# Optimization experiments

Measured on AMD Instinct MI355X. Metric: run time of the kernel, lower is better.

The kernel has to match this reference:

```python
import jax, jax.numpy as jnp
import numpy as np

N, D, H, O, E = 8192, 512, 2048, 512, 8

def setup_inputs() -> dict:
    key = jax.random.key(0)
    ks = jax.random.split(key, 7)
    s = lambda *sh: 1.0 / np.sqrt(sh[-2] if len(sh) > 1 else 1.0)
    x  = jax.random.normal(ks[0], (N, D), dtype=jnp.float32)
    Wr = jax.random.normal(ks[1], (D, E), dtype=jnp.float32) * (1.0 / np.sqrt(D))
    br = jnp.zeros((E,), dtype=jnp.float32)
    W1 = jax.random.normal(ks[2], (E, D, H), dtype=jnp.float32) * (1.0 / np.sqrt(D))
    b1 = jnp.zeros((E, H), dtype=jnp.float32)
    W2 = jax.random.normal(ks[3], (E, H, O), dtype=jnp.float32) * (1.0 / np.sqrt(H))
    b2 = jnp.zeros((E, O), dtype=jnp.float32)
    return {"x": x, "Wr": Wr, "br": br, "W1": W1, "b1": b1, "W2": W2, "b2": b2}


def reference(x, Wr, br, W1, b1, W2, b2):
    # --- supervised router step: Linear -> softmax -> max ---
    router_logits = x @ Wr + br                      # [N, E]
    router_probs = jax.nn.softmax(router_logits, axis=-1)
    p_max = jnp.max(router_probs, axis=-1)           # [N]
    routes = jnp.argmax(router_probs, axis=-1)       # [N] int
    onehot = jax.nn.one_hot(routes, W1.shape[0], dtype=x.dtype)  # [N, E] dispatch mask

    # --- per-expert MLP (dense reference for the gather/compute/scatter pattern) ---
    h = jax.nn.relu(jnp.einsum('nd,edh->enh', x, W1) + b1[:, None, :])  # [E, N, H]
    all_out = jnp.einsum('enh,eho->eno', h, W2) + b2[:, None, :]        # [E, N, O]

    # --- combine: each token takes its routed expert's output ---
    out = jnp.einsum('ne,eno->no', onehot, all_out)  # [N, O]

    # straight-through scaling: value 1 in fwd, routes gradient into router probs
    scale = p_max / jax.lax.stop_gradient(p_max)
    logits = out * scale[:, None]

    counts = jnp.sum(onehot, axis=0)                 # tokens per expert
    return logits, router_probs, counts
```

## Files before the change

### kernel.cpp

```cpp
#include <hip/hip_runtime.h>
#include <hip/hip_bf16.h>
#include <stdint.h>

#define N_TOK 8192
#define DIM   512
#define HID   2048
#define OUTD  512
#define NEXP  8

typedef short  bf16x8 __attribute__((ext_vector_type(8)));
typedef float  f32x4  __attribute__((ext_vector_type(4)));
typedef unsigned short u16x8 __attribute__((ext_vector_type(8)));

#define WS_CNT    0
#define WS_LIST   4096
#define WS_XBF    266240
#define WS_W1T    8654848
#define WS_W2T    25432064
#define WS_H      42209280

__device__ __forceinline__ unsigned short f2bf(float f) {
    uint32_t u = __builtin_bit_cast(uint32_t, f);
    u = (u + 0x7fffu + ((u >> 16) & 1u)) >> 16;
    return (unsigned short)u;
}

__device__ __forceinline__ void gload16(const void* g, void* l) {
    __builtin_amdgcn_global_load_lds(
        (const __attribute__((address_space(1))) unsigned int*)g,
        (__attribute__((address_space(3))) unsigned int*)l, 16, 0, 0);
}

#define MFMA_BF16 __builtin_amdgcn_mfma_f32_16x16x32_bf16

__global__ __launch_bounds__(256) void k1_kernel(
    const float* __restrict__ x, const float* __restrict__ wr, const float* __restrict__ br,
    const float* __restrict__ w1,
    float* __restrict__ probs, int* __restrict__ cnt, int* __restrict__ list,
    unsigned short* __restrict__ xbf, unsigned short* __restrict__ w1t)
{
    const int bid = blockIdx.x, tid = threadIdx.x;
    if (bid < 256) {
        __shared__ int lcnt[NEXP], lbase[NEXP];
        __shared__ int am_l[32], slot_l[32];
        const int w = tid >> 6, lane = tid & 63;
        if (tid < NEXP) lcnt[tid] = 0;
        __syncthreads();
        for (int i = 0; i < 8; i++) {
            const int n = bid * 32 + w * 8 + i;
            float acc[NEXP] = {};
            #pragma unroll
            for (int db = 0; db < 8; db++) {
                const int d = db * 64 + lane;
                const float xv = x[(size_t)n * DIM + d];
                const f32x4 wv0 = *(const f32x4*)&wr[d * 8];
                const f32x4 wv1 = *(const f32x4*)&wr[d * 8 + 4];
                #pragma unroll
                for (int e = 0; e < 4; e++) { acc[e] += xv * wv0[e]; acc[4 + e] += xv * wv1[e]; }
            }
            #pragma unroll
            for (int m = 1; m < 64; m <<= 1)
                #pragma unroll
                for (int e = 0; e < NEXP; e++) acc[e] += __shfl_xor(acc[e], m, 64);
            #pragma unroll
            for (int e = 0; e < NEXP; e++) acc[e] += br[e];
            float mx = acc[0]; int am = 0;
            #pragma unroll
            for (int e = 1; e < NEXP; e++) if (acc[e] > mx) { mx = acc[e]; am = e; }
            float p[NEXP]; float s = 0.f;
            #pragma unroll
            for (int e = 0; e < NEXP; e++) { p[e] = expf(acc[e] - mx); s += p[e]; }
            const float inv = 1.f / s;
            if (lane == 0) {
                f32x4 p0, p1;
                #pragma unroll
                for (int e = 0; e < 4; e++) { p0[e] = p[e] * inv; p1[e] = p[e + 4] * inv; }
                *(f32x4*)&probs[(size_t)n * NEXP]     = p0;
                *(f32x4*)&probs[(size_t)n * NEXP + 4] = p1;
                const int slot = atomicAdd(&lcnt[am], 1);
                am_l[w * 8 + i] = am; slot_l[w * 8 + i] = slot;
            }
        }
        __syncthreads();
        if (tid < NEXP) lbase[tid] = atomicAdd(&cnt[tid], lcnt[tid]);
        __syncthreads();
        if (tid < 32) {
            const int a = am_l[tid];
            list[a * N_TOK + lbase[a] + slot_l[tid]] = bid * 32 + tid;
        }
        const int row = bid * 32 + (tid >> 3), seg = tid & 7;
        const float* src = x + (size_t)row * DIM + seg * 64;
        unsigned short* dst = xbf + (size_t)row * DIM + seg * 64;
        #pragma unroll
        for (int j = 0; j < 8; j++) {
            f32x4 a = *(const f32x4*)&src[j * 8];
            f32x4 b = *(const f32x4*)&src[j * 8 + 4];
            u16x8 o;
            #pragma unroll
            for (int q2 = 0; q2 < 4; q2++) { o[q2] = f2bf(a[q2]); o[4 + q2] = f2bf(b[q2]); }
            *(u16x8*)&dst[j * 8] = o;
        }
    } else {
        __shared__ float t[64][65];
        const int loc = bid - 256, e = loc >> 8, l2 = loc & 255;
        const float* pin = w1 + (size_t)e * DIM * HID;
        unsigned short* pout = w1t + (size_t)e * DIM * HID;
        const int r0 = (l2 >> 5) * 64, c0 = (l2 & 31) * 64;
        const int r = tid >> 2, q = tid & 3;
        #pragma unroll
        for (int j = 0; j < 4; j++) {
            f32x4 v = *(const f32x4*)&pin[(size_t)(r0 + r) * HID + c0 + q * 16 + j * 4];
            #pragma unroll
            for (int i = 0; i < 4; i++) t[r][q * 16 + j * 4 + i] = v[i];
        }
        __syncthreads();
        unsigned short o[16];
        #pragma unroll
        for (int i = 0; i < 16; i++) o[i] = f2bf(t[q * 16 + i][r]);
        unsigned short* dst = &pout[(size_t)(c0 + r) * DIM + r0 + q * 16];
        *(u16x8*)dst       = *(const u16x8*)&o[0];
        *(u16x8*)(dst + 8) = *(const u16x8*)&o[8];
    }
}

__device__ __forceinline__ int xcd_swizzle(int bid, int nwg, bool& valid) {
    const int xcd = bid & 7, cidx = bid >> 3;
    const int q = nwg >> 3, r = nwg & 7;
    const int csz = q + (xcd < r ? 1 : 0);
    valid = (cidx < csz);
    return (xcd < r ? xcd * (q + 1) : r * (q + 1) + (xcd - r) * q) + cidx;
}

__device__ __forceinline__ void tile_map128(const int* __restrict__ cnt, int tile,
                                            int& e, int& row0, int& bs, int& m_e, int& ntiles) {
    int c[NEXP]; ntiles = 0;
    #pragma unroll
    for (int i = 0; i < NEXP; i++) { c[i] = cnt[i]; ntiles += (c[i] + 127) >> 7; }
    int t = tile, b = 0, ei = 0;
    #pragma unroll
    for (int i = 0; i < NEXP; i++) {
        const int nt = (c[i] + 127) >> 7;
        if (t >= 0 && t < nt) { ei = i; row0 = t << 7; bs = b; m_e = c[i]; }
        t -= nt; b += c[i];
    }
    e = ei;
}

#define G1_TILES 2272

__global__ __launch_bounds__(256) void gemmB_kernel(
    const unsigned short* __restrict__ xbf, const unsigned short* __restrict__ w1t,
    const float* __restrict__ b1, const int* __restrict__ list,
    const int* __restrict__ cnt, unsigned short* __restrict__ h,
    const float* __restrict__ w2, unsigned short* __restrict__ w2t)
{
    __shared__ char smem[25088] __attribute__((aligned(16)));
    const int bid = blockIdx.x, tid = threadIdx.x;
    int role, idx;
    if (bid < 4096) { role = (bid >> 3) & 1; idx = ((bid >> 4) << 3) | (bid & 7); }
    else            { role = 0; idx = 2048 + (bid - 4096); }

    if (role == 1) {
        float (*t)[65] = (float(*)[65])smem;
        const int e = idx >> 8, l2 = idx & 255;
        const float* pin = w2 + (size_t)e * HID * OUTD;
        unsigned short* pout = w2t + (size_t)e * HID * OUTD;
        const int r0 = (l2 >> 3) * 64, c0 = (l2 & 7) * 64;
        const int r = tid >> 2, q = tid & 3;
        #pragma unroll
        for (int j = 0; j < 4; j++) {
            f32x4 v = *(const f32x4*)&pin[(size_t)(r0 + r) * OUTD + c0 + q * 16 + j * 4];
            #pragma unroll
            for (int i = 0; i < 4; i++) t[r][q * 16 + j * 4 + i] = v[i];
        }
        __syncthreads();
        unsigned short o[16];
        #pragma unroll
        for (int i = 0; i < 16; i++) o[i] = f2bf(t[q * 16 + i][r]);
        unsigned short* dst = &pout[(size_t)(c0 + r) * HID + r0 + q * 16];
        *(u16x8*)dst       = *(const u16x8*)&o[0];
        *(u16x8*)(dst + 8) = *(const u16x8*)&o[8];
        return;
    }

    unsigned short* ldsA = (unsigned short*)smem;
    unsigned short* ldsB = (unsigned short*)(smem + 16384);
    int* ldsTok = (int*)(smem + 24576);

    int e = 0, row0 = 0, bs = 0, m_e = 0, ntm = 0;
    tile_map128(cnt, 0, e, row0, bs, m_e, ntm);
    const int nwg = ntm * 32;
    bool valid; const int v = xcd_swizzle(idx, nwg, valid);
    if (!valid) return;
    const int tile = v >> 5, ntile = v & 31;
    tile_map128(cnt, tile, e, row0, bs, m_e, ntm);
    const int n0 = ntile * 64;

    if (tid < 128) { int r = row0 + tid; if (r >= m_e) r = m_e - 1; ldsTok[tid] = list[e * N_TOK + r]; }
    __syncthreads();

    const int gslot = tid & 7;
    const unsigned short* aSrc[4]; const unsigned short* bSrc[2];
    #pragma unroll
    for (int i = 0; i < 4; i++) {
        const int row = (i * 256 + tid) >> 3;
        const int col = ((gslot ^ (row & 7)) << 3);
        aSrc[i] = xbf + (size_t)ldsTok[row] * DIM + col;
    }
    #pragma unroll
    for (int i = 0; i < 2; i++) {
        const int row = (i * 256 + tid) >> 3;
        const int col = ((gslot ^ (row & 7)) << 3);
        bSrc[i] = w1t + ((size_t)e * HID + n0 + row) * DIM + col;
    }

    f32x4 acc[4][2] = {};
    const int lane = tid & 63, wid = tid >> 6;
    const int wm = (wid >> 1) * 64, wn = (wid & 1) * 32;
    const int lrow = lane & 15, gk = lane >> 4, lm = lrow & 7;

    int rowA[4], rowB[2];
    #pragma unroll
    for (int f = 0; f < 4; f++) rowA[f] = (wm + f * 16 + lrow) * 64;
    #pragma unroll
    for (int f = 0; f < 2; f++) rowB[f] = (wn + f * 16 + lrow) * 64;

    for (int t = 0; t < 8; t++) {
        const int k0 = t * 64;
        __syncthreads();
        #pragma unroll
        for (int i = 0; i < 4; i++)
            gload16(aSrc[i] + k0, ldsA + ((i << 8) + (tid & 192)) * 8);
        #pragma unroll
        for (int i = 0; i < 2; i++)
            gload16(bSrc[i] + k0, ldsB + ((i << 8) + (tid & 192)) * 8);
        __syncthreads();
        #pragma unroll
        for (int kk = 0; kk < 2; kk++) {
            bf16x8 av[4], bv[2];
            #pragma unroll
            for (int f = 0; f < 4; f++)
                av[f] = *(const bf16x8*)&ldsA[rowA[f] + ((((kk << 2) + gk) ^ lm) << 3)];
            #pragma unroll
            for (int f = 0; f < 2; f++)
                bv[f] = *(const bf16x8*)&ldsB[rowB[f] + ((((kk << 2) + gk) ^ lm) << 3)];
            #pragma unroll
            for (int mf = 0; mf < 4; mf++)
                #pragma unroll
                for (int nf = 0; nf < 2; nf++)
                    acc[mf][nf] = MFMA_BF16(av[mf], bv[nf], acc[mf][nf], 0, 0, 0);
        }
    }

    const int hbase = bs + row0;
    float bias[2];
    #pragma unroll
    for (int nf = 0; nf < 2; nf++) bias[nf] = b1[e * HID + n0 + wn + nf * 16 + lrow];
    #pragma unroll
    for (int mf = 0; mf < 4; mf++) {
        #pragma unroll
        for (int j = 0; j < 4; j++) {
            const int m = wm + mf * 16 + gk * 4 + j;
            if (row0 + m < m_e) {
                const size_t ro = (size_t)(hbase + m) * HID + n0 + wn;
                #pragma unroll
                for (int nf = 0; nf < 2; nf++) {
                    float vv = acc[mf][nf][j] + bias[nf];
                    h[ro + nf * 16 + lrow] = f2bf(vv > 0.f ? vv : 0.f);
                }
            }
        }
    }
}

__global__ __launch_bounds__(256) void gemm2_kernel(
    const unsigned short* __restrict__ h, const unsigned short* __restrict__ w2t,
    const float* __restrict__ b2, const int* __restrict__ list,
    const int* __restrict__ cnt, float* __restrict__ out, float* __restrict__ counts)
{
    const int tid = threadIdx.x;
    if (blockIdx.x == 0 && tid < NEXP) counts[tid] = (float)cnt[tid];

    int e = 0, row0 = 0, bs = 0, m_e = 0, ntm = 0;
    tile_map128(cnt, 0, e, row0, bs, m_e, ntm);
    const int nwg = ntm * 8;
    bool valid; const int v = xcd_swizzle(blockIdx.x, nwg, valid);
    if (!valid) return;
    const int tile = v >> 3, ntile = v & 7;
    tile_map128(cnt, tile, e, row0, bs, m_e, ntm);
    const int n0 = ntile * 64;

    __shared__ unsigned short ldsA[128 * 64] __attribute__((aligned(16)));
    __shared__ unsigned short ldsB[64 * 64]  __attribute__((aligned(16)));
    __shared__ int ldsTok[128];
    if (tid < 128) { int r = row0 + tid; if (r >= m_e) r = m_e - 1; ldsTok[tid] = list[e * N_TOK + r]; }
    __syncthreads();

    const int gslot = tid & 7;
    const unsigned short* aSrc[4]; const unsigned short* bSrc[2];
    #pragma unroll
    for (int i = 0; i < 4; i++) {
        const int row = (i * 256 + tid) >> 3;
        const int col = ((gslot ^ (row & 7)) << 3);
        int slot = row0 + row; if (slot >= m_e) slot = m_e - 1;
        aSrc[i] = h + (size_t)(bs + slot) * HID + col;
    }
    #pragma unroll
    for (int i = 0; i < 2; i++) {
        const int row = (i * 256 + tid) >> 3;
        const int col = ((gslot ^ (row & 7)) << 3);
        bSrc[i] = w2t + ((size_t)e * OUTD + n0 + row) * HID + col;
    }

    f32x4 acc[4][2] = {};
    const int lane = tid & 63, wid = tid >> 6;
    const int wm = (wid >> 1) * 64, wn = (wid & 1) * 32;
    const int lrow = lane & 15, gk = lane >> 4, lm = lrow & 7;

    int rowA[4], rowB[2];
    #pragma unroll
    for (int f = 0; f < 4; f++) rowA[f] = (wm + f * 16 + lrow) * 64;
    #pragma unroll
    for (int f = 0; f < 2; f++) rowB[f] = (wn + f * 16 + lrow) * 64;

    for (int t = 0; t < 32; t++) {
        const int k0 = t * 64;
        __syncthreads();
        #pragma unroll
        for (int i = 0; i < 4; i++)
            gload16(aSrc[i] + k0, ldsA + ((i << 8) + (tid & 192)) * 8);
        #pragma unroll
        for (int i = 0; i < 2; i++)
            gload16(bSrc[i] + k0, ldsB + ((i << 8) + (tid & 192)) * 8);
        __syncthreads();
        #pragma unroll
        for (int kk = 0; kk < 2; kk++) {
            bf16x8 av[4], bv[2];
            #pragma unroll
            for (int f = 0; f < 4; f++)
                av[f] = *(const bf16x8*)&ldsA[rowA[f] + ((((kk << 2) + gk) ^ lm) << 3)];
            #pragma unroll
            for (int f = 0; f < 2; f++)
                bv[f] = *(const bf16x8*)&ldsB[rowB[f] + ((((kk << 2) + gk) ^ lm) << 3)];
            #pragma unroll
            for (int mf = 0; mf < 4; mf++)
                #pragma unroll
                for (int nf = 0; nf < 2; nf++)
                    acc[mf][nf] = MFMA_BF16(av[mf], bv[nf], acc[mf][nf], 0, 0, 0);
        }
    }

    float bias[2];
    #pragma unroll
    for (int nf = 0; nf < 2; nf++) bias[nf] = b2[e * OUTD + n0 + wn + nf * 16 + lrow];
    #pragma unroll
    for (int mf = 0; mf < 4; mf++) {
        #pragma unroll
        for (int j = 0; j < 4; j++) {
            const int m = wm + mf * 16 + gk * 4 + j;
            if (row0 + m < m_e) {
                const size_t ro = (size_t)ldsTok[m] * OUTD + n0 + wn;
                #pragma unroll
                for (int nf = 0; nf < 2; nf++)
                    out[ro + nf * 16 + lrow] = acc[mf][nf][j] + bias[nf];
            }
        }
    }
}

extern "C" void kernel_launch(void* const* d_in, const int* in_sizes, int n_in,
                              void* d_out, int out_size, void* d_ws, size_t ws_size,
                              hipStream_t stream) {
    (void)in_sizes; (void)n_in; (void)out_size; (void)ws_size;
    const float* x  = (const float*)d_in[0];
    const float* wr = (const float*)d_in[1];
    const float* br = (const float*)d_in[2];
    const float* w1 = (const float*)d_in[3];
    const float* b1 = (const float*)d_in[4];
    const float* w2 = (const float*)d_in[5];
    const float* b2 = (const float*)d_in[6];

    float* out    = (float*)d_out;
    float* probs  = out + (size_t)N_TOK * OUTD;
    float* counts = probs + (size_t)N_TOK * NEXP;

    char* ws = (char*)d_ws;
    int* cnt     = (int*)(ws + WS_CNT);
    int* list    = (int*)(ws + WS_LIST);
    unsigned short* xbf = (unsigned short*)(ws + WS_XBF);
    unsigned short* w1t = (unsigned short*)(ws + WS_W1T);
    unsigned short* w2t = (unsigned short*)(ws + WS_W2T);
    unsigned short* hbf = (unsigned short*)(ws + WS_H);

    hipMemsetAsync(cnt, 0, NEXP * sizeof(int), stream);
    k1_kernel<<<2304, 256, 0, stream>>>(x, wr, br, w1, probs, cnt, list, xbf, w1t);
    gemmB_kernel<<<4320, 256, 0, stream>>>(xbf, w1t, b1, list, cnt, hbf, w2, w2t);
    gemm2_kernel<<<568, 256, 0, stream>>>(hbf, w2t, b2, list, cnt, out, counts);
}
```

Before: 111.3 us.

## Double K-tile depth in gemm2 and reorder gemmB block roles

gemm2 now stages 128-wide K slices instead of 64, using a 16-way XOR swizzle with contiguous LDS writes. That halves the number of barrier-separated load/compute iterations at the cost of twice the LDS (about 48KB), which may reduce occupancy. gemmB no longer interleaves W2-transpose blocks with GEMM1 blocks: all GEMM blocks come first and the transpose blocks follow, which changes when each kind of work gets scheduled. A shared swizzle offset is also hoisted in the gemmB inner loop.

Result: faster. 101.5 us, median of 3 (-8.8%).

```diff
diff --git a/kernel.cpp b/kernel.cpp
--- a/kernel.cpp
+++ b/kernel.cpp
@@ -146,7 +146,7 @@
     e = ei;
 }
 
-#define G1_TILES 2272
+#define G1_GRID 2272
 
 __global__ __launch_bounds__(256) void gemmB_kernel(
     const unsigned short* __restrict__ xbf, const unsigned short* __restrict__ w1t,
@@ -155,14 +155,11 @@
     const float* __restrict__ w2, unsigned short* __restrict__ w2t)
 {
     __shared__ char smem[25088] __attribute__((aligned(16)));
-    const int bid = blockIdx.x, tid = threadIdx.x;
-    int role, idx;
-    if (bid < 4096) { role = (bid >> 3) & 1; idx = ((bid >> 4) << 3) | (bid & 7); }
-    else            { role = 0; idx = 2048 + (bid - 4096); }
-
-    if (role == 1) {
+    const int tid = threadIdx.x;
+
+    if ((int)blockIdx.x >= G1_GRID) {
         float (*t)[65] = (float(*)[65])smem;
-        const int e = idx >> 8, l2 = idx & 255;
+        const int loc = blockIdx.x - G1_GRID, e = loc >> 8, l2 = loc & 255;
         const float* pin = w2 + (size_t)e * HID * OUTD;
         unsigned short* pout = w2t + (size_t)e * HID * OUTD;
         const int r0 = (l2 >> 3) * 64, c0 = (l2 & 7) * 64;
@@ -190,7 +187,7 @@
     int e = 0, row0 = 0, bs = 0, m_e = 0, ntm = 0;
     tile_map128(cnt, 0, e, row0, bs, m_e, ntm);
     const int nwg = ntm * 32;
-    bool valid; const int v = xcd_swizzle(idx, nwg, valid);
+    bool valid; const int v = xcd_swizzle(blockIdx.x, nwg, valid);
     if (!valid) return;
     const int tile = v >> 5, ntile = v & 31;
     tile_map128(cnt, tile, e, row0, bs, m_e, ntm);
@@ -237,13 +234,14 @@
         __syncthreads();
         #pragma unroll
         for (int kk = 0; kk < 2; kk++) {
+            const int gsel = (((kk << 2) + gk) ^ lm) << 3;
             bf16x8 av[4], bv[2];
             #pragma unroll
             for (int f = 0; f < 4; f++)
-                av[f] = *(const bf16x8*)&ldsA[rowA[f] + ((((kk << 2) + gk) ^ lm) << 3)];
+                av[f] = *(const bf16x8*)&ldsA[rowA[f] + gsel];
             #pragma unroll
             for (int f = 0; f < 2; f++)
-                bv[f] = *(const bf16x8*)&ldsB[rowB[f] + ((((kk << 2) + gk) ^ lm) << 3)];
+                bv[f] = *(const bf16x8*)&ldsB[rowB[f] + gsel];
             #pragma unroll
             for (int mf = 0; mf < 4; mf++)
                 #pragma unroll
@@ -290,58 +288,56 @@
     tile_map128(cnt, tile, e, row0, bs, m_e, ntm);
     const int n0 = ntile * 64;
 
-    __shared__ unsigned short ldsA[128 * 64] __attribute__((aligned(16)));
-    __shared__ unsigned short ldsB[64 * 64]  __attribute__((aligned(16)));
+    __shared__ unsigned short ldsA[128 * 128] __attribute__((aligned(16)));
+    __shared__ unsigned short ldsB[64 * 128]  __attribute__((aligned(16)));
     __shared__ int ldsTok[128];
     if (tid < 128) { int r = row0 + tid; if (r >= m_e) r = m_e - 1; ldsTok[tid] = list[e * N_TOK + r]; }
     __syncthreads();
 
-    const int gslot = tid & 7;
-    const unsigned short* aSrc[4]; const unsigned short* bSrc[2];
+    const unsigned short* aSrc[8]; const unsigned short* bSrc[4];
+    #pragma unroll
+    for (int i = 0; i < 8; i++) {
+        const int g = i * 256 + tid, row = g >> 4, gc = g & 15;
+        int slot = row0 + row; if (slot >= m_e) slot = m_e - 1;
+        aSrc[i] = h + (size_t)(bs + slot) * HID + ((gc ^ (row & 15)) << 3);
+    }
     #pragma unroll
     for (int i = 0; i < 4; i++) {
-        const int row = (i * 256 + tid) >> 3;
-        const int col = ((gslot ^ (row & 7)) << 3);
-        int slot = row0 + row; if (slot >= m_e) slot = m_e - 1;
-        aSrc[i] = h + (size_t)(bs + slot) * HID + col;
-    }
-    #pragma unroll
-    for (int i = 0; i < 2; i++) {
-        const int row = (i * 256 + tid) >> 3;
-        const int col = ((gslot ^ (row & 7)) << 3);
-        bSrc[i] = w2t + ((size_t)e * OUTD + n0 + row) * HID + col;
+        const int g = i * 256 + tid, row = g >> 4, gc = g & 15;
+        bSrc[i] = w2t + ((size_t)e * OUTD + n0 + row) * HID + ((gc ^ (row & 15)) << 3);
     }
 
     f32x4 acc[4][2] = {};
     const int lane = tid & 63, wid = tid >> 6;
     const int wm = (wid >> 1) * 64, wn = (wid & 1) * 32;
-    const int lrow = lane & 15, gk = lane >> 4, lm = lrow & 7;
+    const int lrow = lane & 15, gk = lane >> 4;
 
     int rowA[4], rowB[2];
     #pragma unroll
-    for (int f = 0; f < 4; f++) rowA[f] = (wm + f * 16 + lrow) * 64;
-    #pragma unroll
-    for (int f = 0; f < 2; f++) rowB[f] = (wn + f * 16 + lrow) * 64;
-
-    for (int t = 0; t < 32; t++) {
-        const int k0 = t * 64;
-        __syncthreads();
+    for (int f = 0; f < 4; f++) rowA[f] = (wm + f * 16 + lrow) * 128;
+    #pragma unroll
+    for (int f = 0; f < 2; f++) rowB[f] = (wn + f * 16 + lrow) * 128;
+
+    for (int t = 0; t < 16; t++) {
+        const int k0 = t * 128;
+        __syncthreads();
+        #pragma unroll
+        for (int i = 0; i < 8; i++)
+            gload16(aSrc[i] + k0, ldsA + (i * 256 + tid) * 8);
         #pragma unroll
         for (int i = 0; i < 4; i++)
-            gload16(aSrc[i] + k0, ldsA + ((i << 8) + (tid & 192)) * 8);
-        #pragma unroll
-        for (int i = 0; i < 2; i++)
-            gload16(bSrc[i] + k0, ldsB + ((i << 8) + (tid & 192)) * 8);
-        __syncthreads();
-        #pragma unroll
-        for (int kk = 0; kk < 2; kk++) {
+            gload16(bSrc[i] + k0, ldsB + (i * 256 + tid) * 8);
+        __syncthreads();
+        #pragma unroll
+        for (int kk = 0; kk < 4; kk++) {
+            const int gsel = (((kk << 2) + gk) ^ lrow) << 3;
             bf16x8 av[4], bv[2];
             #pragma unroll
             for (int f = 0; f < 4; f++)
-                av[f] = *(const bf16x8*)&ldsA[rowA[f] + ((((kk << 2) + gk) ^ lm) << 3)];
+                av[f] = *(const bf16x8*)&ldsA[rowA[f] + gsel];
             #pragma unroll
             for (int f = 0; f < 2; f++)
-                bv[f] = *(const bf16x8*)&ldsB[rowB[f] + ((((kk << 2) + gk) ^ lm) << 3)];
+                bv[f] = *(const bf16x8*)&ldsB[rowB[f] + gsel];
             #pragma unroll
             for (int mf = 0; mf < 4; mf++)
                 #pragma unroll
@@ -394,6 +390,6 @@
 
     hipMemsetAsync(cnt, 0, NEXP * sizeof(int), stream);
     k1_kernel<<<2304, 256, 0, stream>>>(x, wr, br, w1, probs, cnt, list, xbf, w1t);
-    gemmB_kernel<<<4320, 256, 0, stream>>>(xbf, w1t, b1, list, cnt, hbf, w2, w2t);
+    gemmB_kernel<<<G1_GRID + 2048, 256, 0, stream>>>(xbf, w1t, b1, list, cnt, hbf, w2, w2t);
     gemm2_kernel<<<568, 256, 0, stream>>>(hbf, w2t, b2, list, cnt, out, counts);
 }
```
